# Kernel tuning notes

Hardware: AMD Instinct MI355X
Metric: run time of the kernel (lower is better)

Reference implementation:

```python
import jax, jax.numpy as jnp
import numpy as np

T, H, I, E = 1024, 2048, 3200, 8  # tokens, hidden, intermediate, experts
JITTER_EPS = 0.01


def sparsemixer(scores, jitter_eps=JITTER_EPS):
    # ---- top-1 ----
    max1 = jnp.max(scores, axis=-1, keepdims=True)
    ind1 = jnp.argmax(scores, axis=-1, keepdims=True)  # first-max, matches torch
    factor = jnp.maximum(jnp.abs(scores), max1)        # clamp(min=max1)
    mask = (max1 - scores) / factor > 2.0 * jitter_eps
    masked_gates = jax.nn.softmax(jnp.where(mask, -jnp.inf, scores), axis=-1)
    mult1 = jnp.take_along_axis(masked_gates, ind1, axis=-1)
    # ---- mask out top-1, then top-2 ----
    top1_onehot = jax.nn.one_hot(ind1[..., 0], scores.shape[-1], dtype=bool)
    masked_scores = jnp.where(top1_onehot, -jnp.inf, scores)
    max2 = jnp.max(masked_scores, axis=-1, keepdims=True)
    ind2 = jnp.argmax(masked_scores, axis=-1, keepdims=True)
    factor2 = jnp.maximum(jnp.abs(scores), max2)
    mask2 = (max2 - scores) / factor2 > 2.0 * jitter_eps
    masked_gates2 = jax.nn.softmax(jnp.where(mask2, -jnp.inf, masked_scores), axis=-1)
    mult2 = jnp.take_along_axis(masked_gates2, ind2, axis=-1)
    multiplier = jnp.concatenate([mult1, mult2], axis=-1)       # [T, 2]
    selected = jnp.concatenate([ind1, ind2], axis=-1)           # [T, 2] int
    return multiplier, selected


def setup_inputs() -> dict:
    key = jax.random.key(0)
    k0, k1, k2, k3, k4 = jax.random.split(key, 5)
    hidden_states = jax.random.normal(k0, (T, H), dtype=jnp.float32)
    gate_w = jax.random.normal(k1, (E, H), dtype=jnp.float32) * (H ** -0.5)
    w1 = jax.random.normal(k2, (E, I, H), dtype=jnp.float32) * (H ** -0.5)
    w3 = jax.random.normal(k3, (E, I, H), dtype=jnp.float32) * (H ** -0.5)
    w2 = jax.random.normal(k4, (E, H, I), dtype=jnp.float32) * (I ** -0.5)
    return {"hidden_states": hidden_states, "gate_w": gate_w,
            "w1": w1, "w3": w3, "w2": w2}


def reference(hidden_states, gate_w, w1, w3, w2):
    x = hidden_states.reshape(-1, gate_w.shape[1])              # [T, H]
    router_logits = x @ gate_w.T                                # [T, E]
    topk_w, topk_ids = sparsemixer(router_logits)               # [T,2], [T,2]
    n_exp = gate_w.shape[0]
    # combine top-2 (weight, id) pairs into a dense [T, E] gate matrix
    gates = jnp.sum(jax.nn.one_hot(topk_ids, n_exp, dtype=x.dtype)
                    * topk_w[..., None], axis=1)                # [T, E]
    # SiLU-gated expert MLPs, combined with routing gates
    h1 = jnp.einsum('th,eih->tei', x, w1)                       # [T, E, I]
    h3 = jnp.einsum('th,eih->tei', x, w3)
    act = jax.nn.silu(h1) * h3                                  # [T, E, I]
    out = jnp.einsum('tei,ehi,te->th', act, w2, gates)          # [T, H]
    return out.reshape(hidden_states.shape)
```

## Files before the change

kernel.cpp:

```cpp
#include <hip/hip_runtime.h>

#define T_ 1024
#define H_ 2048
#define I_ 3200
#define E_ 8

typedef float fvec4 __attribute__((ext_vector_type(4)));
typedef float f32x4 __attribute__((ext_vector_type(4)));
typedef __bf16 bf16x8 __attribute__((ext_vector_type(8)));
typedef unsigned short u16x4 __attribute__((ext_vector_type(4)));

typedef const __attribute__((address_space(1))) void* gp1_t;
typedef __attribute__((address_space(3))) void* sp3_t;

#define WS_CHUNK 128
#define WS_TOK   512
#define WS_GATE  33280
#define WS_XB    66560
#define WS_ACT   4261888
#define MAXCH    16

#define BARX() { asm volatile("s_waitcnt lgkmcnt(0)" ::: "memory"); \
    __builtin_amdgcn_sched_barrier(0); __builtin_amdgcn_s_barrier(); \
    __builtin_amdgcn_sched_barrier(0); }
#define BAR1() { __builtin_amdgcn_sched_barrier(0); __builtin_amdgcn_s_barrier(); \
    __builtin_amdgcn_sched_barrier(0); }

__global__ __launch_bounds__(256) void router_kernel(const float* __restrict__ x,
                                                     const float* __restrict__ gw,
                                                     int* __restrict__ cnt,
                                                     int* __restrict__ tok,
                                                     float* __restrict__ gate,
                                                     unsigned short* __restrict__ xb) {
  const int lane = threadIdx.x & 63;
  const int wv = threadIdx.x >> 6;
  const int t = blockIdx.x * 4 + wv;

  const float* xp = x + (size_t)t * H_;
  fvec4 xr[8];
#pragma unroll
  for (int j = 0; j < 8; ++j) xr[j] = *(const fvec4*)(xp + j * 256 + lane * 4);

  unsigned short* xbp = xb + (size_t)t * H_;
#pragma unroll
  for (int j = 0; j < 8; ++j) {
    u16x4 o;
#pragma unroll
    for (int c = 0; c < 4; ++c) o[c] = __builtin_bit_cast(unsigned short, (__bf16)xr[j][c]);
    *(u16x4*)(xbp + j * 256 + lane * 4) = o;
  }

  float s[E_];
#pragma unroll
  for (int e = 0; e < E_; ++e) {
    const float* gp = gw + (size_t)e * H_;
    float p = 0.f;
#pragma unroll
    for (int j = 0; j < 8; ++j) {
      fvec4 g = *(const fvec4*)(gp + j * 256 + lane * 4);
      p = fmaf(xr[j][0], g[0], p); p = fmaf(xr[j][1], g[1], p);
      p = fmaf(xr[j][2], g[2], p); p = fmaf(xr[j][3], g[3], p);
    }
#pragma unroll
    for (int off = 32; off > 0; off >>= 1) p += __shfl_xor(p, off);
    s[e] = p;
  }

  float max1 = s[0]; int i1 = 0;
#pragma unroll
  for (int e = 1; e < E_; ++e) if (s[e] > max1) { max1 = s[e]; i1 = e; }
  float den1 = 0.f;
#pragma unroll
  for (int e = 0; e < E_; ++e) {
    float factor = fmaxf(fabsf(s[e]), max1);
    if ((max1 - s[e]) <= 0.02f * factor) den1 += expf(s[e] - max1);
  }
  float mult1 = 1.f / den1;

  float max2 = -INFINITY; int i2 = 0;
#pragma unroll
  for (int e = 0; e < E_; ++e) if (e != i1 && s[e] > max2) { max2 = s[e]; i2 = e; }
  float den2 = 0.f;
#pragma unroll
  for (int e = 0; e < E_; ++e) {
    if (e == i1) continue;
    float factor = fmaxf(fabsf(s[e]), max2);
    if ((max2 - s[e]) <= 0.02f * factor) den2 += expf(s[e] - max2);
  }
  float mult2 = 1.f / den2;

  if (lane == 0) {
    int p1 = atomicAdd(&cnt[i1], 1); tok[i1 * T_ + p1] = t; gate[i1 * T_ + p1] = mult1;
    int p2 = atomicAdd(&cnt[i2], 1); tok[i2 * T_ + p2] = t; gate[i2 * T_ + p2] = mult2;
  }
}

__global__ void prefix_kernel(const int* __restrict__ cnt, int* __restrict__ base,
                              int* __restrict__ chunk) {
  if (threadIdx.x == 0 && blockIdx.x == 0) {
    int a = 0, c = 0;
    for (int e = 0; e < E_; ++e) {
      base[e] = a;
      int pc = (cnt[e] + 127) & ~127;
      for (int m = 0; m < pc; m += 256) { chunk[1 + c] = e; chunk[1 + MAXCH + c] = m; ++c; }
      a += pc;
    }
    base[E_] = a;
    chunk[0] = c;
  }
}

__global__ __launch_bounds__(512, 4) void ffn1_kernel(
    const unsigned short* __restrict__ xb, const float* __restrict__ w1,
    const float* __restrict__ w3, const int* __restrict__ cnt,
    const int* __restrict__ base, const int* __restrict__ chunk,
    const int* __restrict__ tokl, unsigned short* __restrict__ actb) {
  if ((int)blockIdx.y >= chunk[0]) return;
  const int e = chunk[1 + blockIdx.y];
  const int m_base = chunk[1 + MAXCH + blockIdx.y];
  const int ab = base[e];
  const int count = cnt[e];
  const int n0 = blockIdx.x * 32;
  const int tid = threadIdx.x;
  const int lane = tid & 63, wv = tid >> 6;
  const int wm = wv >> 1, wn = wv & 1;

  __shared__ unsigned short Ab0[256 * 64];
  __shared__ unsigned short Ab1[256 * 64];
  __shared__ unsigned short B1s[2][32 * 64];
  __shared__ unsigned short B3s[2][32 * 64];

  const unsigned short* aSrc[4];
  const int colg = ((lane & 7) ^ ((lane >> 3) & 7)) * 8;
#pragma unroll
  for (int i = 0; i < 4; ++i) {
    int r = m_base + wv * 32 + i * 8 + (lane >> 3);
    if (r >= count) r = count - 1;
    aSrc[i] = xb + (size_t)tokl[e * T_ + r] * H_ + colg;
  }
  const int brow = tid >> 4, w = tid & 15;
  const float* b1p = w1 + ((size_t)e * I_ + n0 + brow) * H_ + w * 4;
  const float* b3p = w3 + ((size_t)e * I_ + n0 + brow) * H_ + w * 4;
  const int wbyte = brow * 128 + ((((w >> 1)) ^ (brow & 7)) << 4) + (w & 1) * 8;

  f32x4 acc1[4], acc3[4];
#pragma unroll
  for (int mi = 0; mi < 4; ++mi) { acc1[mi] = (f32x4){0,0,0,0}; acc3[mi] = (f32x4){0,0,0,0}; }

  auto STAGE_A = [&](unsigned short* dst, int kb) {
#pragma unroll
    for (int i = 0; i < 4; ++i)
      __builtin_amdgcn_global_load_lds((gp1_t)(aSrc[i] + kb),
                                       (sp3_t)(dst + (wv * 32 + i * 8) * 64), 16, 0, 0);
  };
  auto LOADB = [&](fvec4& r1, fvec4& r3, int kb) {
    r1 = *(const fvec4*)(b1p + kb);
    r3 = *(const fvec4*)(b3p + kb);
  };
  auto CVTW = [&](fvec4& r1, fvec4& r3, int buf) {
    u16x4 v, u;
#pragma unroll
    for (int c = 0; c < 4; ++c) {
      v[c] = __builtin_bit_cast(unsigned short, (__bf16)r1[c]);
      u[c] = __builtin_bit_cast(unsigned short, (__bf16)r3[c]);
    }
    *(u16x4*)((char*)B1s[buf] + wbyte) = v;
    *(u16x4*)((char*)B3s[buf] + wbyte) = u;
  };
  auto STEP = [&](const unsigned short* A_, int bbuf) {
#pragma unroll
    for (int kk = 0; kk < 2; ++kk) {
      const int c16 = kk * 4 + (lane >> 4);
      bf16x8 af[4];
#pragma unroll
      for (int mi = 0; mi < 4; ++mi) {
        int ar = wm * 64 + mi * 16 + (lane & 15);
        af[mi] = *(const bf16x8*)((const char*)A_ + ar * 128 + ((c16 ^ (ar & 7)) << 4));
      }
      int br = wn * 16 + (lane & 15);
      bf16x8 f1 = *(const bf16x8*)((const char*)B1s[bbuf] + br * 128 + ((c16 ^ (br & 7)) << 4));
      bf16x8 f3 = *(const bf16x8*)((const char*)B3s[bbuf] + br * 128 + ((c16 ^ (br & 7)) << 4));
      __builtin_amdgcn_s_setprio(1);
#pragma unroll
      for (int mi = 0; mi < 4; ++mi) {
        acc1[mi] = __builtin_amdgcn_mfma_f32_16x16x32_bf16(af[mi], f1, acc1[mi], 0, 0, 0);
        acc3[mi] = __builtin_amdgcn_mfma_f32_16x16x32_bf16(af[mi], f3, acc3[mi], 0, 0, 0);
      }
      __builtin_amdgcn_s_setprio(0);
    }
  };

  const int NT = H_ / 64;
  fvec4 ra1, ra3, rb1, rb3;

  STAGE_A(Ab0, 0);  LOADB(ra1, ra3, 0);
  STAGE_A(Ab1, 64); LOADB(rb1, rb3, 64);
  asm volatile("s_waitcnt vmcnt(6)" ::: "memory");
  CVTW(ra1, ra3, 0);
  LOADB(ra1, ra3, 128);
  BARX();

  for (int t = 0; t < NT; t += 2) {
    STEP(Ab0, 0);
    BAR1();
    if (t + 2 < NT) {
      STAGE_A(Ab0, (t + 2) * 64);
      asm volatile("s_waitcnt vmcnt(6)" ::: "memory");
    } else {
      asm volatile("s_waitcnt vmcnt(0)" ::: "memory");
    }
    CVTW(rb1, rb3, 1);
    if (t + 3 < NT) LOADB(rb1, rb3, (t + 3) * 64);
    BARX();
    STEP(Ab1, 1);
    if (t + 2 >= NT) break;
    BAR1();
    if (t + 3 < NT) {
      STAGE_A(Ab1, (t + 3) * 64);
      asm volatile("s_waitcnt vmcnt(6)" ::: "memory");
    } else {
      asm volatile("s_waitcnt vmcnt(0)" ::: "memory");
    }
    CVTW(ra1, ra3, 0);
    if (t + 4 < NT) LOADB(ra1, ra3, (t + 4) * 64);
    BARX();
  }

  const int row_lim = (base[e + 1] - ab) - m_base;
#pragma unroll
  for (int mi = 0; mi < 4; ++mi)
#pragma unroll
    for (int j = 0; j < 4; ++j) {
      int row = wm * 64 + mi * 16 + (lane >> 4) * 4 + j;
      if (row < row_lim) {
        float h1 = acc1[mi][j];
        float a = (h1 / (1.f + __expf(-h1))) * acc3[mi][j];
        actb[(size_t)(ab + m_base + row) * I_ + n0 + wn * 16 + (lane & 15)] =
            __builtin_bit_cast(unsigned short, (__bf16)a);
      }
    }
}

__global__ __launch_bounds__(512, 4) void ffn2_kernel(
    const unsigned short* __restrict__ actb, const float* __restrict__ w2,
    const int* __restrict__ cnt, const int* __restrict__ base,
    const int* __restrict__ chunk, const int* __restrict__ tokl,
    const float* __restrict__ gatel, float* __restrict__ out) {
  if ((int)blockIdx.y >= chunk[0]) return;
  const int e = chunk[1 + blockIdx.y];
  const int m_base = chunk[1 + MAXCH + blockIdx.y];
  const int count = cnt[e];
  if (m_base >= count) return;
  const int ab = base[e];
  const int n0 = blockIdx.x * 32;
  const int tid = threadIdx.x;
  const int lane = tid & 63, wv = tid >> 6;
  const int wm = wv >> 1, wn = wv & 1;

  __shared__ unsigned short Ab0[256 * 64];
  __shared__ unsigned short Ab1[256 * 64];
  __shared__ unsigned short Bs[2][32 * 64];

  const unsigned short* aSrc[4];
  const int colg = ((lane & 7) ^ ((lane >> 3) & 7)) * 8;
#pragma unroll
  for (int i = 0; i < 4; ++i) {
    int r = ab + m_base + wv * 32 + i * 8 + (lane >> 3);
    aSrc[i] = actb + (size_t)r * I_ + colg;
  }
  const int brow = tid >> 4, w = tid & 15;
  const float* bp = w2 + ((size_t)e * H_ + n0 + brow) * I_ + w * 4;
  const int wbyte = brow * 128 + ((((w >> 1)) ^ (brow & 7)) << 4) + (w & 1) * 8;

  f32x4 acc[4];
#pragma unroll
  for (int mi = 0; mi < 4; ++mi) acc[mi] = (f32x4){0,0,0,0};

  auto STAGE_A = [&](unsigned short* dst, int kb) {
#pragma unroll
    for (int i = 0; i < 4; ++i)
      __builtin_amdgcn_global_load_lds((gp1_t)(aSrc[i] + kb),
                                       (sp3_t)(dst + (wv * 32 + i * 8) * 64), 16, 0, 0);
  };
  auto LOADB = [&](fvec4& r, int kb) { r = *(const fvec4*)(bp + kb); };
  auto CVTW = [&](fvec4& r, int buf) {
    u16x4 v;
#pragma unroll
    for (int c = 0; c < 4; ++c) v[c] = __builtin_bit_cast(unsigned short, (__bf16)r[c]);
    *(u16x4*)((char*)Bs[buf] + wbyte) = v;
  };
  auto STEP = [&](const unsigned short* A_, int bbuf) {
#pragma unroll
    for (int kk = 0; kk < 2; ++kk) {
      const int c16 = kk * 4 + (lane >> 4);
      bf16x8 af[4];
#pragma unroll
      for (int mi = 0; mi < 4; ++mi) {
        int ar = wm * 64 + mi * 16 + (lane & 15);
        af[mi] = *(const bf16x8*)((const char*)A_ + ar * 128 + ((c16 ^ (ar & 7)) << 4));
      }
      int br = wn * 16 + (lane & 15);
      bf16x8 f = *(const bf16x8*)((const char*)Bs[bbuf] + br * 128 + ((c16 ^ (br & 7)) << 4));
      __builtin_amdgcn_s_setprio(1);
#pragma unroll
      for (int mi = 0; mi < 4; ++mi)
        acc[mi] = __builtin_amdgcn_mfma_f32_16x16x32_bf16(af[mi], f, acc[mi], 0, 0, 0);
      __builtin_amdgcn_s_setprio(0);
    }
  };

  const int NT = I_ / 64;
  fvec4 ra, rb;

  STAGE_A(Ab0, 0);  LOADB(ra, 0);
  STAGE_A(Ab1, 64); LOADB(rb, 64);
  asm volatile("s_waitcnt vmcnt(5)" ::: "memory");
  CVTW(ra, 0);
  LOADB(ra, 128);
  BARX();

  for (int t = 0; t < NT; t += 2) {
    STEP(Ab0, 0);
    BAR1();
    if (t + 2 < NT) {
      STAGE_A(Ab0, (t + 2) * 64);
      asm volatile("s_waitcnt vmcnt(5)" ::: "memory");
    } else {
      asm volatile("s_waitcnt vmcnt(0)" ::: "memory");
    }
    CVTW(rb, 1);
    if (t + 3 < NT) LOADB(rb, (t + 3) * 64);
    BARX();
    STEP(Ab1, 1);
    if (t + 2 >= NT) break;
    BAR1();
    if (t + 3 < NT) {
      STAGE_A(Ab1, (t + 3) * 64);
      asm volatile("s_waitcnt vmcnt(5)" ::: "memory");
    } else {
      asm volatile("s_waitcnt vmcnt(0)" ::: "memory");
    }
    CVTW(ra, 0);
    if (t + 4 < NT) LOADB(ra, (t + 4) * 64);
    BARX();
  }

#pragma unroll
  for (int mi = 0; mi < 4; ++mi)
#pragma unroll
    for (int j = 0; j < 4; ++j) {
      int row = m_base + wm * 64 + mi * 16 + (lane >> 4) * 4 + j;
      if (row < count) {
        int tokv = tokl[e * T_ + row];
        float g = gatel[e * T_ + row];
        atomicAdd(&out[(size_t)tokv * H_ + n0 + wn * 16 + (lane & 15)], g * acc[mi][j]);
      }
    }
}

extern "C" void kernel_launch(void* const* d_in, const int* in_sizes, int n_in,
                              void* d_out, int out_size, void* d_ws, size_t ws_size,
                              hipStream_t stream) {
  const float* x  = (const float*)d_in[0];
  const float* gw = (const float*)d_in[1];
  const float* w1 = (const float*)d_in[2];
  const float* w3 = (const float*)d_in[3];
  const float* w2 = (const float*)d_in[4];
  float* out = (float*)d_out;
  char* ws = (char*)d_ws;

  int* cnt = (int*)ws;
  int* base = (int*)(ws + 64);
  int* chunk = (int*)(ws + WS_CHUNK);
  int* tokl = (int*)(ws + WS_TOK);
  float* gatel = (float*)(ws + WS_GATE);
  unsigned short* xb = (unsigned short*)(ws + WS_XB);
  unsigned short* actb = (unsigned short*)(ws + WS_ACT);

  (void)hipMemsetAsync(d_out, 0, (size_t)T_ * H_ * sizeof(float), stream);
  (void)hipMemsetAsync(ws, 0, 64, stream);

  router_kernel<<<T_ / 4, 256, 0, stream>>>(x, gw, cnt, tokl, gatel, xb);
  prefix_kernel<<<1, 64, 0, stream>>>(cnt, base, chunk);
  ffn1_kernel<<<dim3(I_ / 32, MAXCH), 512, 0, stream>>>(xb, w1, w3, cnt, base, chunk, tokl, actb);
  ffn2_kernel<<<dim3(H_ / 32, MAXCH), 512, 0, stream>>>(actb, w2, cnt, base, chunk, tokl, gatel, out);
}
```

Before: 339.6 us.

## Convert FFN kernels to persistent work-stealing with single-barrier double-buffered pipeline

Both FFN GEMM kernels now launch a fixed grid of 512 persistent blocks. Each block pulls (chunk, column-tile) work items from an atomic counter, so the many empty blocks of the old MAXCH-sized grid no longer get scheduled. The main loop is also rewritten from a two-step unrolled loop with two barriers per step into a one-tile-per-iteration double buffer with a single barrier. Only one A tile is prefetched ahead, so there is less latency hiding. Each item also pays extra __syncthreads and an atomic, and the counters rely on the existing 64-byte workspace memset.

After: 446.2 us. +31.4%, slower.

```diff
diff --git a/kernel.cpp b/kernel.cpp
--- a/kernel.cpp
+++ b/kernel.cpp
@@ -22,8 +22,6 @@
 
 #define BARX() { asm volatile("s_waitcnt lgkmcnt(0)" ::: "memory"); \
     __builtin_amdgcn_sched_barrier(0); __builtin_amdgcn_s_barrier(); \
-    __builtin_amdgcn_sched_barrier(0); }
-#define BAR1() { __builtin_amdgcn_sched_barrier(0); __builtin_amdgcn_s_barrier(); \
     __builtin_amdgcn_sched_barrier(0); }
 
 __global__ __launch_bounds__(256) void router_kernel(const float* __restrict__ x,
@@ -114,248 +112,243 @@
     const unsigned short* __restrict__ xb, const float* __restrict__ w1,
     const float* __restrict__ w3, const int* __restrict__ cnt,
     const int* __restrict__ base, const int* __restrict__ chunk,
-    const int* __restrict__ tokl, unsigned short* __restrict__ actb) {
-  if ((int)blockIdx.y >= chunk[0]) return;
-  const int e = chunk[1 + blockIdx.y];
-  const int m_base = chunk[1 + MAXCH + blockIdx.y];
-  const int ab = base[e];
-  const int count = cnt[e];
-  const int n0 = blockIdx.x * 32;
+    const int* __restrict__ tokl, unsigned short* __restrict__ actb,
+    int* __restrict__ wk) {
   const int tid = threadIdx.x;
   const int lane = tid & 63, wv = tid >> 6;
   const int wm = wv >> 1, wn = wv & 1;
 
-  __shared__ unsigned short Ab0[256 * 64];
-  __shared__ unsigned short Ab1[256 * 64];
+  __shared__ unsigned short Ab[2][256 * 64];
   __shared__ unsigned short B1s[2][32 * 64];
   __shared__ unsigned short B3s[2][32 * 64];
-
-  const unsigned short* aSrc[4];
+  __shared__ int sItem;
+
+  const int nwork = chunk[0] * 100;
+  const int brow = tid >> 4, w = tid & 15;
+  const int wbyte = brow * 128 + (((w >> 1) ^ (brow & 7)) << 4) + (w & 1) * 8;
   const int colg = ((lane & 7) ^ ((lane >> 3) & 7)) * 8;
-#pragma unroll
-  for (int i = 0; i < 4; ++i) {
-    int r = m_base + wv * 32 + i * 8 + (lane >> 3);
-    if (r >= count) r = count - 1;
-    aSrc[i] = xb + (size_t)tokl[e * T_ + r] * H_ + colg;
-  }
-  const int brow = tid >> 4, w = tid & 15;
-  const float* b1p = w1 + ((size_t)e * I_ + n0 + brow) * H_ + w * 4;
-  const float* b3p = w3 + ((size_t)e * I_ + n0 + brow) * H_ + w * 4;
-  const int wbyte = brow * 128 + ((((w >> 1)) ^ (brow & 7)) << 4) + (w & 1) * 8;
-
-  f32x4 acc1[4], acc3[4];
-#pragma unroll
-  for (int mi = 0; mi < 4; ++mi) { acc1[mi] = (f32x4){0,0,0,0}; acc3[mi] = (f32x4){0,0,0,0}; }
-
-  auto STAGE_A = [&](unsigned short* dst, int kb) {
-#pragma unroll
-    for (int i = 0; i < 4; ++i)
-      __builtin_amdgcn_global_load_lds((gp1_t)(aSrc[i] + kb),
-                                       (sp3_t)(dst + (wv * 32 + i * 8) * 64), 16, 0, 0);
-  };
-  auto LOADB = [&](fvec4& r1, fvec4& r3, int kb) {
-    r1 = *(const fvec4*)(b1p + kb);
-    r3 = *(const fvec4*)(b3p + kb);
-  };
-  auto CVTW = [&](fvec4& r1, fvec4& r3, int buf) {
-    u16x4 v, u;
-#pragma unroll
-    for (int c = 0; c < 4; ++c) {
-      v[c] = __builtin_bit_cast(unsigned short, (__bf16)r1[c]);
-      u[c] = __builtin_bit_cast(unsigned short, (__bf16)r3[c]);
-    }
-    *(u16x4*)((char*)B1s[buf] + wbyte) = v;
-    *(u16x4*)((char*)B3s[buf] + wbyte) = u;
-  };
-  auto STEP = [&](const unsigned short* A_, int bbuf) {
-#pragma unroll
-    for (int kk = 0; kk < 2; ++kk) {
-      const int c16 = kk * 4 + (lane >> 4);
-      bf16x8 af[4];
-#pragma unroll
-      for (int mi = 0; mi < 4; ++mi) {
-        int ar = wm * 64 + mi * 16 + (lane & 15);
-        af[mi] = *(const bf16x8*)((const char*)A_ + ar * 128 + ((c16 ^ (ar & 7)) << 4));
-      }
-      int br = wn * 16 + (lane & 15);
-      bf16x8 f1 = *(const bf16x8*)((const char*)B1s[bbuf] + br * 128 + ((c16 ^ (br & 7)) << 4));
-      bf16x8 f3 = *(const bf16x8*)((const char*)B3s[bbuf] + br * 128 + ((c16 ^ (br & 7)) << 4));
-      __builtin_amdgcn_s_setprio(1);
-#pragma unroll
-      for (int mi = 0; mi < 4; ++mi) {
-        acc1[mi] = __builtin_amdgcn_mfma_f32_16x16x32_bf16(af[mi], f1, acc1[mi], 0, 0, 0);
-        acc3[mi] = __builtin_amdgcn_mfma_f32_16x16x32_bf16(af[mi], f3, acc3[mi], 0, 0, 0);
-      }
-      __builtin_amdgcn_s_setprio(0);
-    }
-  };
-
   const int NT = H_ / 64;
-  fvec4 ra1, ra3, rb1, rb3;
-
-  STAGE_A(Ab0, 0);  LOADB(ra1, ra3, 0);
-  STAGE_A(Ab1, 64); LOADB(rb1, rb3, 64);
-  asm volatile("s_waitcnt vmcnt(6)" ::: "memory");
-  CVTW(ra1, ra3, 0);
-  LOADB(ra1, ra3, 128);
-  BARX();
-
-  for (int t = 0; t < NT; t += 2) {
-    STEP(Ab0, 0);
-    BAR1();
-    if (t + 2 < NT) {
-      STAGE_A(Ab0, (t + 2) * 64);
-      asm volatile("s_waitcnt vmcnt(6)" ::: "memory");
-    } else {
-      asm volatile("s_waitcnt vmcnt(0)" ::: "memory");
-    }
-    CVTW(rb1, rb3, 1);
-    if (t + 3 < NT) LOADB(rb1, rb3, (t + 3) * 64);
+
+  for (;;) {
+    __syncthreads();
+    if (tid == 0) sItem = atomicAdd(wk, 1);
+    __syncthreads();
+    const int item = sItem;
+    if (item >= nwork) return;
+    const int c = item / 100;
+    const int n0 = (item - c * 100) * 32;
+    const int e = chunk[1 + c];
+    const int m_base = chunk[1 + MAXCH + c];
+    const int ab = base[e];
+    const int count = cnt[e];
+
+    const unsigned short* aSrc[4];
+#pragma unroll
+    for (int i = 0; i < 4; ++i) {
+      int r = m_base + wv * 32 + i * 8 + (lane >> 3);
+      if (r >= count) r = count - 1;
+      aSrc[i] = xb + (size_t)tokl[e * T_ + r] * H_ + colg;
+    }
+    const float* b1p = w1 + ((size_t)e * I_ + n0 + brow) * H_ + w * 4;
+    const float* b3p = w3 + ((size_t)e * I_ + n0 + brow) * H_ + w * 4;
+
+    f32x4 acc1[4], acc3[4];
+#pragma unroll
+    for (int mi = 0; mi < 4; ++mi) { acc1[mi] = (f32x4){0,0,0,0}; acc3[mi] = (f32x4){0,0,0,0}; }
+
+    auto STAGE_A = [&](unsigned short* dst, int kb) {
+#pragma unroll
+      for (int i = 0; i < 4; ++i)
+        __builtin_amdgcn_global_load_lds((gp1_t)(aSrc[i] + kb),
+                                         (sp3_t)(dst + (wv * 32 + i * 8) * 64), 16, 0, 0);
+    };
+    auto LOADB = [&](fvec4& r1, fvec4& r3, int kb) {
+      r1 = *(const fvec4*)(b1p + kb);
+      r3 = *(const fvec4*)(b3p + kb);
+    };
+    auto CVTW = [&](fvec4& r1, fvec4& r3, int buf) {
+      u16x4 v, u;
+#pragma unroll
+      for (int cc = 0; cc < 4; ++cc) {
+        v[cc] = __builtin_bit_cast(unsigned short, (__bf16)r1[cc]);
+        u[cc] = __builtin_bit_cast(unsigned short, (__bf16)r3[cc]);
+      }
+      *(u16x4*)((char*)B1s[buf] + wbyte) = v;
+      *(u16x4*)((char*)B3s[buf] + wbyte) = u;
+    };
+    auto STEP = [&](const unsigned short* A_, int bbuf) {
+#pragma unroll
+      for (int kk = 0; kk < 2; ++kk) {
+        const int c16 = kk * 4 + (lane >> 4);
+        bf16x8 af[4];
+#pragma unroll
+        for (int mi = 0; mi < 4; ++mi) {
+          int ar = wm * 64 + mi * 16 + (lane & 15);
+          af[mi] = *(const bf16x8*)((const char*)A_ + ar * 128 + ((c16 ^ (ar & 7)) << 4));
+        }
+        int br = wn * 16 + (lane & 15);
+        bf16x8 f1 = *(const bf16x8*)((const char*)B1s[bbuf] + br * 128 + ((c16 ^ (br & 7)) << 4));
+        bf16x8 f3 = *(const bf16x8*)((const char*)B3s[bbuf] + br * 128 + ((c16 ^ (br & 7)) << 4));
+        __builtin_amdgcn_s_setprio(1);
+#pragma unroll
+        for (int mi = 0; mi < 4; ++mi) {
+          acc1[mi] = __builtin_amdgcn_mfma_f32_16x16x32_bf16(af[mi], f1, acc1[mi], 0, 0, 0);
+          acc3[mi] = __builtin_amdgcn_mfma_f32_16x16x32_bf16(af[mi], f3, acc3[mi], 0, 0, 0);
+        }
+        __builtin_amdgcn_s_setprio(0);
+      }
+    };
+
+    fvec4 ra1, ra3, rb1, rb3;
+    STAGE_A(Ab[0], 0);
+    LOADB(ra1, ra3, 0);
+    LOADB(rb1, rb3, 64);
+    asm volatile("s_waitcnt vmcnt(2)" ::: "memory");
+    CVTW(ra1, ra3, 0);
+    LOADB(ra1, ra3, 128);
     BARX();
-    STEP(Ab1, 1);
-    if (t + 2 >= NT) break;
-    BAR1();
-    if (t + 3 < NT) {
-      STAGE_A(Ab1, (t + 3) * 64);
-      asm volatile("s_waitcnt vmcnt(6)" ::: "memory");
-    } else {
-      asm volatile("s_waitcnt vmcnt(0)" ::: "memory");
-    }
-    CVTW(ra1, ra3, 0);
-    if (t + 4 < NT) LOADB(ra1, ra3, (t + 4) * 64);
-    BARX();
-  }
-
-  const int row_lim = (base[e + 1] - ab) - m_base;
-#pragma unroll
-  for (int mi = 0; mi < 4; ++mi)
-#pragma unroll
-    for (int j = 0; j < 4; ++j) {
-      int row = wm * 64 + mi * 16 + (lane >> 4) * 4 + j;
-      if (row < row_lim) {
-        float h1 = acc1[mi][j];
-        float a = (h1 / (1.f + __expf(-h1))) * acc3[mi][j];
-        actb[(size_t)(ab + m_base + row) * I_ + n0 + wn * 16 + (lane & 15)] =
-            __builtin_bit_cast(unsigned short, (__bf16)a);
-      }
-    }
+
+    for (int t = 0; t < NT; ++t) {
+      const int cur = t & 1;
+      if (t + 1 < NT) STAGE_A(Ab[cur ^ 1], (t + 1) * 64);
+      STEP(Ab[cur], cur);
+      if (t + 1 < NT) {
+        if (cur == 0) { CVTW(rb1, rb3, 1); if (t + 3 < NT) LOADB(rb1, rb3, (t + 3) * 64); }
+        else          { CVTW(ra1, ra3, 0); if (t + 3 < NT) LOADB(ra1, ra3, (t + 3) * 64); }
+      }
+      if (t + 2 < NT) { asm volatile("s_waitcnt vmcnt(2)" ::: "memory"); }
+      else            { asm volatile("s_waitcnt vmcnt(0)" ::: "memory"); }
+      BARX();
+    }
+
+    const int row_lim = (base[e + 1] - ab) - m_base;
+#pragma unroll
+    for (int mi = 0; mi < 4; ++mi)
+#pragma unroll
+      for (int j = 0; j < 4; ++j) {
+        int row = wm * 64 + mi * 16 + (lane >> 4) * 4 + j;
+        if (row < row_lim) {
+          float h1 = acc1[mi][j];
+          float a = (h1 / (1.f + __expf(-h1))) * acc3[mi][j];
+          actb[(size_t)(ab + m_base + row) * I_ + n0 + wn * 16 + (lane & 15)] =
+              __builtin_bit_cast(unsigned short, (__bf16)a);
+        }
+      }
+  }
 }
 
 __global__ __launch_bounds__(512, 4) void ffn2_kernel(
     const unsigned short* __restrict__ actb, const float* __restrict__ w2,
     const int* __restrict__ cnt, const int* __restrict__ base,
     const int* __restrict__ chunk, const int* __restrict__ tokl,
-    const float* __restrict__ gatel, float* __restrict__ out) {
-  if ((int)blockIdx.y >= chunk[0]) return;
-  const int e = chunk[1 + blockIdx.y];
-  const int m_base = chunk[1 + MAXCH + blockIdx.y];
-  const int count = cnt[e];
-  if (m_base >= count) return;
-  const int ab = base[e];
-  const int n0 = blockIdx.x * 32;
+    const float* __restrict__ gatel, float* __restrict__ out,
+    int* __restrict__ wk) {
   const int tid = threadIdx.x;
   const int lane = tid & 63, wv = tid >> 6;
   const int wm = wv >> 1, wn = wv & 1;
 
-  __shared__ unsigned short Ab0[256 * 64];
-  __shared__ unsigned short Ab1[256 * 64];
+  __shared__ unsigned short Ab[2][256 * 64];
   __shared__ unsigned short Bs[2][32 * 64];
-
-  const unsigned short* aSrc[4];
+  __shared__ int sItem;
+
+  const int nwork = chunk[0] * 64;
+  const int brow = tid >> 4, w = tid & 15;
+  const int wbyte = brow * 128 + (((w >> 1) ^ (brow & 7)) << 4) + (w & 1) * 8;
   const int colg = ((lane & 7) ^ ((lane >> 3) & 7)) * 8;
-#pragma unroll
-  for (int i = 0; i < 4; ++i) {
-    int r = ab + m_base + wv * 32 + i * 8 + (lane >> 3);
-    aSrc[i] = actb + (size_t)r * I_ + colg;
-  }
-  const int brow = tid >> 4, w = tid & 15;
-  const float* bp = w2 + ((size_t)e * H_ + n0 + brow) * I_ + w * 4;
-  const int wbyte = brow * 128 + ((((w >> 1)) ^ (brow & 7)) << 4) + (w & 1) * 8;
-
-  f32x4 acc[4];
-#pragma unroll
-  for (int mi = 0; mi < 4; ++mi) acc[mi] = (f32x4){0,0,0,0};
-
-  auto STAGE_A = [&](unsigned short* dst, int kb) {
-#pragma unroll
-    for (int i = 0; i < 4; ++i)
-      __builtin_amdgcn_global_load_lds((gp1_t)(aSrc[i] + kb),
-                                       (sp3_t)(dst + (wv * 32 + i * 8) * 64), 16, 0, 0);
-  };
-  auto LOADB = [&](fvec4& r, int kb) { r = *(const fvec4*)(bp + kb); };
-  auto CVTW = [&](fvec4& r, int buf) {
-    u16x4 v;
-#pragma unroll
-    for (int c = 0; c < 4; ++c) v[c] = __builtin_bit_cast(unsigned short, (__bf16)r[c]);
-    *(u16x4*)((char*)Bs[buf] + wbyte) = v;
-  };
-  auto STEP = [&](const unsigned short* A_, int bbuf) {
-#pragma unroll
-    for (int kk = 0; kk < 2; ++kk) {
-      const int c16 = kk * 4 + (lane >> 4);
-      bf16x8 af[4];
-#pragma unroll
-      for (int mi = 0; mi < 4; ++mi) {
-        int ar = wm * 64 + mi * 16 + (lane & 15);
-        af[mi] = *(const bf16x8*)((const char*)A_ + ar * 128 + ((c16 ^ (ar & 7)) << 4));
-      }
-      int br = wn * 16 + (lane & 15);
-      bf16x8 f = *(const bf16x8*)((const char*)Bs[bbuf] + br * 128 + ((c16 ^ (br & 7)) << 4));
-      __builtin_amdgcn_s_setprio(1);
-#pragma unroll
-      for (int mi = 0; mi < 4; ++mi)
-        acc[mi] = __builtin_amdgcn_mfma_f32_16x16x32_bf16(af[mi], f, acc[mi], 0, 0, 0);
-      __builtin_amdgcn_s_setprio(0);
-    }
-  };
-
   const int NT = I_ / 64;
-  fvec4 ra, rb;
-
-  STAGE_A(Ab0, 0);  LOADB(ra, 0);
-  STAGE_A(Ab1, 64); LOADB(rb, 64);
-  asm volatile("s_waitcnt vmcnt(5)" ::: "memory");
-  CVTW(ra, 0);
-  LOADB(ra, 128);
-  BARX();
-
-  for (int t = 0; t < NT; t += 2) {
-    STEP(Ab0, 0);
-    BAR1();
-    if (t + 2 < NT) {
-      STAGE_A(Ab0, (t + 2) * 64);
-      asm volatile("s_waitcnt vmcnt(5)" ::: "memory");
-    } else {
-      asm volatile("s_waitcnt vmcnt(0)" ::: "memory");
-    }
-    CVTW(rb, 1);
-    if (t + 3 < NT) LOADB(rb, (t + 3) * 64);
+
+  for (;;) {
+    __syncthreads();
+    if (tid == 0) sItem = atomicAdd(wk, 1);
+    __syncthreads();
+    const int item = sItem;
+    if (item >= nwork) return;
+    const int c = item >> 6;
+    const int n0 = (item & 63) * 32;
+    const int e = chunk[1 + c];
+    const int m_base = chunk[1 + MAXCH + c];
+    const int ab = base[e];
+    const int count = cnt[e];
+
+    const unsigned short* aSrc[4];
+#pragma unroll
+    for (int i = 0; i < 4; ++i) {
+      int r = ab + m_base + wv * 32 + i * 8 + (lane >> 3);
+      aSrc[i] = actb + (size_t)r * I_ + colg;
+    }
+    const float* bp = w2 + ((size_t)e * H_ + n0 + brow) * I_ + w * 4;
+
+    f32x4 acc[4];
+#pragma unroll
+    for (int mi = 0; mi < 4; ++mi) acc[mi] = (f32x4){0,0,0,0};
+
+    auto STAGE_A = [&](unsigned short* dst, int kb) {
+#pragma unroll
+      for (int i = 0; i < 4; ++i)
+        __builtin_amdgcn_global_load_lds((gp1_t)(aSrc[i] + kb),
+                                         (sp3_t)(dst + (wv * 32 + i * 8) * 64), 16, 0, 0);
+    };
+    auto LOADB = [&](fvec4& r, int kb) { r = *(const fvec4*)(bp + kb); };
+    auto CVTW = [&](fvec4& r, int buf) {
+      u16x4 v;
+#pragma unroll
+      for (int cc = 0; cc < 4; ++cc) v[cc] = __builtin_bit_cast(unsigned short, (__bf16)r[cc]);
+      *(u16x4*)((char*)Bs[buf] + wbyte) = v;
+    };
+    auto STEP = [&](const unsigned short* A_, int bbuf) {
+#pragma unroll
+      for (int kk = 0; kk < 2; ++kk) {
+        const int c16 = kk * 4 + (lane >> 4);
+        bf16x8 af[4];
+#pragma unroll
+        for (int mi = 0; mi < 4; ++mi) {
+          int ar = wm * 64 + mi * 16 + (lane & 15);
+          af[mi] = *(const bf16x8*)((const char*)A_ + ar * 128 + ((c16 ^ (ar & 7)) << 4));
+        }
+        int br = wn * 16 + (lane & 15);
+        bf16x8 f = *(const bf16x8*)((const char*)Bs[bbuf] + br * 128 + ((c16 ^ (br & 7)) << 4));
+        __builtin_amdgcn_s_setprio(1);
+#pragma unroll
+        for (int mi = 0; mi < 4; ++mi)
+          acc[mi] = __builtin_amdgcn_mfma_f32_16x16x32_bf16(af[mi], f, acc[mi], 0, 0, 0);
+        __builtin_amdgcn_s_setprio(0);
+      }
+    };
+
+    fvec4 ra, rb;
+    STAGE_A(Ab[0], 0);
+    LOADB(ra, 0);
+    LOADB(rb, 64);
+    asm volatile("s_waitcnt vmcnt(1)" ::: "memory");
+    CVTW(ra, 0);
+    LOADB(ra, 128);
     BARX();
-    STEP(Ab1, 1);
-    if (t + 2 >= NT) break;
-    BAR1();
-    if (t + 3 < NT) {
-      STAGE_A(Ab1, (t + 3) * 64);
-      asm volatile("s_waitcnt vmcnt(5)" ::: "memory");
-    } else {
-      asm volatile("s_waitcnt vmcnt(0)" ::: "memory");
-    }
-    CVTW(ra, 0);
-    if (t + 4 < NT) LOADB(ra, (t + 4) * 64);
-    BARX();
-  }
-
-#pragma unroll
-  for (int mi = 0; mi < 4; ++mi)
-#pragma unroll
-    for (int j = 0; j < 4; ++j) {
-      int row = m_base + wm * 64 + mi * 16 + (lane >> 4) * 4 + j;
-      if (row < count) {
-        int tokv = tokl[e * T_ + row];
-        float g = gatel[e * T_ + row];
-        atomicAdd(&out[(size_t)tokv * H_ + n0 + wn * 16 + (lane & 15)], g * acc[mi][j]);
-      }
-    }
+
+    for (int t = 0; t < NT; ++t) {
+      const int cur = t & 1;
+      if (t + 1 < NT) STAGE_A(Ab[cur ^ 1], (t + 1) * 64);
+      STEP(Ab[cur], cur);
+      if (t + 1 < NT) {
+        if (cur == 0) { CVTW(rb, 1); if (t + 3 < NT) LOADB(rb, (t + 3) * 64); }
+        else          { CVTW(ra, 0); if (t + 3 < NT) LOADB(ra, (t + 3) * 64); }
+      }
+      if (t + 2 < NT) { asm volatile("s_waitcnt vmcnt(1)" ::: "memory"); }
+      else            { asm volatile("s_waitcnt vmcnt(0)" ::: "memory"); }
+      BARX();
+    }
+
+#pragma unroll
+    for (int mi = 0; mi < 4; ++mi)
+#pragma unroll
+      for (int j = 0; j < 4; ++j) {
+        int row = m_base + wm * 64 + mi * 16 + (lane >> 4) * 4 + j;
+        if (row < count) {
+          int tokv = tokl[e * T_ + row];
+          float g = gatel[e * T_ + row];
+          atomicAdd(&out[(size_t)tokv * H_ + n0 + wn * 16 + (lane & 15)], g * acc[mi][j]);
+        }
+      }
+  }
 }
 
 extern "C" void kernel_launch(void* const* d_in, const int* in_sizes, int n_in,
@@ -370,6 +363,8 @@
   char* ws = (char*)d_ws;
 
   int* cnt = (int*)ws;
+  int* wk1 = (int*)(ws + 32);
+  int* wk2 = (int*)(ws + 36);
   int* base = (int*)(ws + 64);
   int* chunk = (int*)(ws + WS_CHUNK);
   int* tokl = (int*)(ws + WS_TOK);
@@ -382,6 +377,6 @@
 
   router_kernel<<<T_ / 4, 256, 0, stream>>>(x, gw, cnt, tokl, gatel, xb);
   prefix_kernel<<<1, 64, 0, stream>>>(cnt, base, chunk);
-  ffn1_kernel<<<dim3(I_ / 32, MAXCH), 512, 0, stream>>>(xb, w1, w3, cnt, base, chunk, tokl, actb);
-  ffn2_kernel<<<dim3(H_ / 32, MAXCH), 512, 0, stream>>>(actb, w2, cnt, base, chunk, tokl, gatel, out);
-}
+  ffn1_kernel<<<512, 512, 0, stream>>>(xb, w1, w3, cnt, base, chunk, tokl, actb, wk1);
+  ffn2_kernel<<<512, 512, 0, stream>>>(actb, w2, cnt, base, chunk, tokl, gatel, out, wk2);
+}
```
